# Performance work log

Measured on AMD Instinct MI355X. Metric: run time of the kernel, lower is better.

## Reference

```python
import jax, jax.numpy as jnp
import numpy as np

VOCAB = 32000
DIM = 1024
BATCH = 2
SEQ = 2048
CHUNK = 256
LCTX = 4            # local_context_size, mode='sum'
LOCAL_WIN = 512     # sparse_local_window (>= 2*chunk)
GSTRIDE = 1024      # sparse_global_stride (>= 4*chunk)
LN_EPS = 1e-5


def _cache_positions():
    """Simulate the deterministic sparse KV-cache pruning per chunk (numpy, trace-time).
    Returns list of key-position index arrays (cached positions ++ current chunk)."""
    cache = np.zeros((0,), dtype=np.int64)
    per_chunk = []
    for i in range(SEQ // CHUNK):
        new = np.arange(i * CHUNK, (i + 1) * CHUNK, dtype=np.int64)
        full = np.concatenate([cache, new])
        per_chunk.append(full)
        total_seen = (i + 1) * CHUNK
        local_start = max(0, total_seen - LOCAL_WIN)
        keep = (full >= local_start) | (full % GSTRIDE == 0)
        cache = full[keep]
    return per_chunk


def setup_inputs() -> dict:
    key = jax.random.key(0)
    ks = jax.random.split(key, 8)
    s = 0.02
    return {
        "x": jax.random.randint(ks[0], (BATCH, SEQ), 0, VOCAB, dtype=jnp.int64),
        "emb_table": jax.random.normal(ks[1], (VOCAB, DIM), jnp.float32) * s,
        "q_w": jax.random.normal(ks[2], (DIM, DIM), jnp.float32) * s,
        "q_b": jnp.zeros((DIM,), jnp.float32),
        "k_w": jax.random.normal(ks[3], (DIM, DIM), jnp.float32) * s,
        "k_b": jnp.zeros((DIM,), jnp.float32),
        "v_w": jax.random.normal(ks[4], (DIM, DIM), jnp.float32) * s,
        "v_b": jnp.zeros((DIM,), jnp.float32),
        "o_w": jax.random.normal(ks[5], (DIM, DIM), jnp.float32) * s,
        "o_b": jnp.zeros((DIM,), jnp.float32),
        "ln_w": jnp.ones((DIM,), jnp.float32),
        "ln_b": jnp.zeros((DIM,), jnp.float32),
        "out_w": jax.random.normal(ks[6], (VOCAB, DIM), jnp.float32) * s,
        "out_b": jnp.zeros((VOCAB,), jnp.float32),
    }


def reference(x, emb_table, q_w, q_b, k_w, k_b, v_w, v_b, o_w, o_b, ln_w, ln_b, out_w, out_b):
    # embedding + causal local context (sum of 0..LCTX-1 shifted embeddings)
    emb = emb_table[x]                                  # [B,S,D]
    ctx = emb
    for off in range(1, LCTX):
        ctx = ctx + jnp.pad(emb, ((0, 0), (off, 0), (0, 0)))[:, :SEQ]

    # project full sequence once (same per-chunk projections in the original)
    Q = ctx @ q_w.T + q_b                               # [B,S,D]
    K = ctx @ k_w.T + k_b
    V = ctx @ v_w.T + v_b
    scale = 1.0 / np.sqrt(DIM).astype(np.float32)

    outs = []
    for i, kpos in enumerate(_cache_positions()):
        qpos = np.arange(i * CHUNK, (i + 1) * CHUNK, dtype=np.int64)
        q = Q[:, i * CHUNK:(i + 1) * CHUNK]             # [B,C,D]
        k = K[:, kpos]                                  # [B,Ki,D] gathered sparse cache + chunk
        v = V[:, kpos]
        scores = jnp.einsum('bqd,bkd->bqk', q, k) * scale
        mask = kpos[None, :] > qpos[:, None]            # [C,Ki] static causal mask
        scores = jnp.where(mask[None, :, :], -jnp.inf, scores)
        w = jax.nn.softmax(scores, axis=-1)
        outs.append(jnp.einsum('bqk,bkd->bqd', w, v))

    attended = jnp.concatenate(outs, axis=1)            # [B,S,D]
    h = attended @ o_w.T + o_b
    # LayerNorm
    mu = h.mean(-1, keepdims=True)
    var = ((h - mu) ** 2).mean(-1, keepdims=True)
    h = (h - mu) / jnp.sqrt(var + LN_EPS) * ln_w + ln_b
    return h @ out_w.T + out_b                          # [B,S,VOCAB]
```

## Files before the change

kernel.cpp:

```cpp
#include <hip/hip_runtime.h>
#include <stdint.h>

#define DIMN 1024
#define SEQN 2048
#define BATCHN 2
#define NCHUNK 8
#define CHUNKSZ 256
#define VOCABN 32000
#define ROWS_PB 6016
#define PSTRIDE_B (256*ROWS_PB)
#define LN_EPS 1e-5f

#define MBIG 4096
#define NBIG 32000
#define KBIG 1024
#define NTILES_K (KBIG/64)

typedef unsigned short ushort_t;
typedef __attribute__((ext_vector_type(8))) __bf16 bf16x8;
typedef __attribute__((ext_vector_type(4))) float f32x4;

__device__ const int d_nk[8]   = {256,512,768,769,769,769,769,770};
__device__ const int d_np[8]   = {256,512,768,896,896,896,896,896};
__device__ const int d_koff[8] = {0,256,768,1536,2432,3328,4224,5120};

__device__ __forceinline__ ushort_t f2bu(float f) {
  union { float f; unsigned u; } v; v.f = f;
  unsigned r = v.u + 0x7FFFu + ((v.u >> 16) & 1u);
  return (ushort_t)(r >> 16);
}
__device__ __forceinline__ float b2f(ushort_t u) {
  union { unsigned u; float f; } v; v.u = ((unsigned)u) << 16; return v.f;
}

__device__ __forceinline__ int pos_of(int i, int j) {
  if (i <= 2) return j;
  if (i <= 6) return (j == 0) ? 0 : (i - 3) * 256 + 255 + j;
  return (j == 0) ? 0 : ((j == 1) ? 1024 : 1278 + j);
}

__device__ __forceinline__ void gload16(const void* g, void* l) {
  __builtin_amdgcn_global_load_lds((__attribute__((address_space(1))) void*)g,
                                   (__attribute__((address_space(3))) void*)l,
                                   16, 0, 0);
}

__device__ __forceinline__ void mma_core_s(const ushort_t* __restrict__ A,
                                           const ushort_t* __restrict__ Bt,
                                           int K, ushort_t* lA, ushort_t* lB,
                                           f32x4 acc[4][4], int tid) {
  const int lane = tid & 63;
  const int wr = (tid >> 7) & 1;
  const int wc = (tid >> 6) & 1;
  const int frow = lane & 15;
  const int lhi = lane >> 4;
  const int xk = (frow & 7) << 4;
  const size_t ldb = (size_t)K * 2;
  for (int kt = 0; kt < K; kt += 64) {
#pragma unroll
    for (int t = 0; t < 4; ++t) {
      int cid = t * 256 + tid;
      int row = cid >> 3;
      int srcoff = ((cid & 7) * 16) ^ ((row & 7) << 4);
      gload16((const char*)A  + (size_t)row * ldb + (size_t)kt * 2 + srcoff,
              (char*)lA + cid * 16);
      gload16((const char*)Bt + (size_t)row * ldb + (size_t)kt * 2 + srcoff,
              (char*)lB + cid * 16);
    }
    __syncthreads();
#pragma unroll
    for (int kk = 0; kk < 2; ++kk) {
      bf16x8 af[4], bfr[4];
#pragma unroll
      for (int m = 0; m < 4; ++m) {
        int r = wr * 64 + m * 16 + frow;
        af[m] = *(const bf16x8*)((const char*)lA +
                 ((r * 128 + kk * 64 + lhi * 16) ^ xk));
      }
#pragma unroll
      for (int n = 0; n < 4; ++n) {
        int r = wc * 64 + n * 16 + frow;
        bfr[n] = *(const bf16x8*)((const char*)lB +
                  ((r * 128 + kk * 64 + lhi * 16) ^ xk));
      }
#pragma unroll
      for (int m = 0; m < 4; ++m)
#pragma unroll
        for (int n = 0; n < 4; ++n)
          acc[m][n] = __builtin_amdgcn_mfma_f32_16x16x32_bf16(af[m], bfr[n],
                                                              acc[m][n], 0, 0, 0);
    }
    __syncthreads();
  }
}

__device__ __forceinline__ void stage_tile_big(const char* Abase, const char* Bbase,
                                               ushort_t* ldsbuf, int ktile, int tid) {
  const size_t ldb = (size_t)KBIG * 2;
#pragma unroll
  for (int s = 0; s < 4; ++s) {
    const char* base = (s < 2 ? Abase : Bbase) + (size_t)(s & 1) * 128 * ldb
                       + (size_t)ktile * 128;
    ushort_t* lh = ldsbuf + s * 8192;
#pragma unroll
    for (int r2 = 0; r2 < 2; ++r2) {
      int c = r2 * 512 + tid;
      int row = c >> 3;
      int off_l = (c * 16) ^ ((row & 7) << 4);
      gload16(base + (size_t)row * ldb + (off_l & 127), (char*)lh + c * 16);
    }
  }
}

__global__ __launch_bounds__(512, 2) void k_vocab(
    const ushort_t* __restrict__ A, const ushort_t* __restrict__ Bt,
    const float* __restrict__ bias, float* __restrict__ C) {
  __shared__ ushort_t lds[2][4][8192];
  const int tid = threadIdx.x;
  const int lane = tid & 63, w = tid >> 6, wm = w >> 2, wn = w & 3;
  const int frow = lane & 15, lhi = lane >> 4;
  const int xk = (frow & 7) << 4;

  int l = blockIdx.x;
  int swz = (l & 7) * ((int)gridDim.x >> 3) + (l >> 3);
  const int mt = swz & 15;
  const int nt = swz >> 4;
  const char* Abase = (const char*)(A + (size_t)mt * 256 * KBIG);
  const char* Bbase = (const char*)(Bt + (size_t)nt * 256 * KBIG);

  f32x4 acc[8][4] = {};

  stage_tile_big(Abase, Bbase, &lds[0][0][0], 0, tid);

  for (int kt = 0; kt < NTILES_K; ++kt) {
    const int cur = kt & 1;
    __builtin_amdgcn_sched_barrier(0);
    if (kt + 1 < NTILES_K) {
      stage_tile_big(Abase, Bbase, &lds[cur ^ 1][0][0], kt + 1, tid);
      asm volatile("s_waitcnt vmcnt(8)");
    } else {
      asm volatile("s_waitcnt vmcnt(0)");
    }
    __builtin_amdgcn_s_barrier();
    __builtin_amdgcn_sched_barrier(0);

    const char* lA = (const char*)&lds[cur][wm][0];
    const char* lB = (const char*)&lds[cur][2 + (wn >> 1)][0];

    bf16x8 bF[4][2];
#pragma unroll
    for (int fc = 0; fc < 4; ++fc) {
      int c = (wn & 1) * 64 + fc * 16 + frow;
#pragma unroll
      for (int kk = 0; kk < 2; ++kk)
        bF[fc][kk] = *(const bf16x8*)(lB + ((c * 128 + kk * 64 + lhi * 16) ^ xk));
    }
#pragma unroll
    for (int q = 0; q < 4; ++q) {
      bf16x8 aF[2][2];
#pragma unroll
      for (int i = 0; i < 2; ++i) {
        int r = (2 * q + i) * 16 + frow;
#pragma unroll
        for (int kk = 0; kk < 2; ++kk)
          aF[i][kk] = *(const bf16x8*)(lA + ((r * 128 + kk * 64 + lhi * 16) ^ xk));
      }
      if (q) __builtin_amdgcn_s_barrier();
      __builtin_amdgcn_s_setprio(1);
#pragma unroll
      for (int i = 0; i < 2; ++i)
#pragma unroll
        for (int fc = 0; fc < 4; ++fc)
#pragma unroll
          for (int kk = 0; kk < 2; ++kk)
            acc[2 * q + i][fc] = __builtin_amdgcn_mfma_f32_16x16x32_bf16(
                aF[i][kk], bF[fc][kk], acc[2 * q + i][fc], 0, 0, 0);
      __builtin_amdgcn_s_setprio(0);
    }
    __builtin_amdgcn_s_barrier();
  }

  const int rbase = mt * 256 + wm * 128 + lhi * 4;
  const int cbase = nt * 256 + wn * 64 + frow;
#pragma unroll
  for (int fc = 0; fc < 4; ++fc) {
    float bv = bias[cbase + fc * 16];
#pragma unroll
    for (int fr = 0; fr < 8; ++fr)
#pragma unroll
      for (int j = 0; j < 4; ++j)
        C[(size_t)(rbase + fr * 16 + j) * NBIG + cbase + fc * 16] =
            acc[fr][fc][j] + bv;
  }
}

__global__ __launch_bounds__(256) void k_cvt(const float* __restrict__ src,
                                             ushort_t* __restrict__ dst, int n) {
  int idx = blockIdx.x * 256 + threadIdx.x;
  int stride = gridDim.x * 256;
  int n4 = n >> 2;
  for (int i = idx; i < n4; i += stride) {
    float4 v = ((const float4*)src)[i];
    ((ushort4*)dst)[i] = make_ushort4(f2bu(v.x), f2bu(v.y), f2bu(v.z), f2bu(v.w));
  }
}

__global__ __launch_bounds__(256) void k_embed(const int* __restrict__ x,
                                               const float* __restrict__ emb,
                                               ushort_t* __restrict__ ctxb) {
  const int t = blockIdx.x, b = blockIdx.y, tid = threadIdx.x;
  float4 s = make_float4(0.f, 0.f, 0.f, 0.f);
#pragma unroll
  for (int o = 0; o < 4; ++o) {
    if (t - o < 0) break;
    int tok = x[b * SEQN + t - o];
    float4 v = ((const float4*)(emb + (size_t)tok * DIMN))[tid];
    s.x += v.x; s.y += v.y; s.z += v.z; s.w += v.w;
  }
  ((ushort4*)(ctxb + ((size_t)(b * SEQN + t)) * DIMN))[tid] =
      make_ushort4(f2bu(s.x), f2bu(s.y), f2bu(s.z), f2bu(s.w));
}

__global__ __launch_bounds__(256) void k_qkv(const ushort_t* __restrict__ A,
    const ushort_t* __restrict__ Bt, const float* __restrict__ qb2,
    const float* __restrict__ kb2, const float* __restrict__ vb2,
    ushort_t* __restrict__ Qb, ushort_t* __restrict__ Kb,
    ushort_t* __restrict__ Vb) {
  __shared__ __align__(16) ushort_t lA[128*64];
  __shared__ __align__(16) ushort_t lB[128*64];
  f32x4 acc[4][4] = {};
  const int tid = threadIdx.x;
  mma_core_s(A + (size_t)blockIdx.y * 128 * KBIG,
             Bt + (size_t)blockIdx.x * 128 * KBIG, KBIG, lA, lB, acc, tid);
  const int which = blockIdx.x >> 3;
  const int col0  = (blockIdx.x & 7) * 128;
  ushort_t* Out = (which == 0) ? Qb : (which == 1) ? Kb : Vb;
  const float* Bv = (which == 0) ? qb2 : (which == 1) ? kb2 : vb2;
  const int lane = tid & 63, wr = (tid >> 7) & 1, wc = (tid >> 6) & 1;
  const int rbase = blockIdx.y * 128 + wr * 64 + (lane >> 4) * 4;
  const int cbase = col0 + wc * 64 + (lane & 15);
#pragma unroll
  for (int m = 0; m < 4; ++m)
#pragma unroll
    for (int n = 0; n < 4; ++n) {
      int c = cbase + n * 16;
      float bv = Bv[c];
#pragma unroll
      for (int j = 0; j < 4; ++j)
        Out[(size_t)(rbase + m * 16 + j) * DIMN + c] = f2bu(acc[m][n][j] + bv);
    }
}

__global__ __launch_bounds__(256) void k_gemm_f32(const ushort_t* __restrict__ A,
    const ushort_t* __restrict__ Bt, const float* __restrict__ bias,
    float* __restrict__ C, int N, int K) {
  __shared__ __align__(16) ushort_t lA[128*64];
  __shared__ __align__(16) ushort_t lB[128*64];
  f32x4 acc[4][4] = {};
  const int tid = threadIdx.x;
  mma_core_s(A + (size_t)blockIdx.y * 128 * K, Bt + (size_t)blockIdx.x * 128 * K,
             K, lA, lB, acc, tid);
  const int lane = tid & 63, wr = (tid >> 7) & 1, wc = (tid >> 6) & 1;
  const int rbase = blockIdx.y * 128 + wr * 64 + (lane >> 4) * 4;
  const int cbase = blockIdx.x * 128 + wc * 64 + (lane & 15);
#pragma unroll
  for (int m = 0; m < 4; ++m)
#pragma unroll
    for (int n = 0; n < 4; ++n) {
      int c = cbase + n * 16;
      float bv = bias[c];
#pragma unroll
      for (int j = 0; j < 4; ++j)
        C[(size_t)(rbase + m * 16 + j) * N + c] = acc[m][n][j] + bv;
    }
}

__global__ __launch_bounds__(256) void k_gatherK(const ushort_t* __restrict__ Kb,
                                                 ushort_t* __restrict__ Kg) {
  const int r = blockIdx.x, b = blockIdx.y, tid = threadIdx.x;
  int i = 7;
#pragma unroll
  for (int q = 0; q < 7; ++q) if (r < d_koff[q + 1]) { i = q; break; }
  const int j = r - d_koff[i];
  ushort4* dst = (ushort4*)(Kg + ((size_t)b * ROWS_PB + r) * DIMN);
  if (j < d_nk[i]) {
    int pos = pos_of(i, j);
    dst[tid] = ((const ushort4*)(Kb + ((size_t)b * SEQN + pos) * DIMN))[tid];
  } else {
    dst[tid] = make_ushort4(0, 0, 0, 0);
  }
}

__global__ __launch_bounds__(256) void k_transV(const ushort_t* __restrict__ Vb,
                                                ushort_t* __restrict__ VgT) {
  __shared__ ushort_t tile[64][66];
  const int z = blockIdx.z, b = z >> 3, i = z & 7;
  const int np = d_np[i], nk = d_nk[i], ko = d_koff[i];
  const int jb = blockIdx.x * 64;
  if (jb >= np) return;
  const int db = blockIdx.y * 64;
  const int tid = threadIdx.x, tx = tid & 63, ty = tid >> 6;
#pragma unroll
  for (int rep = 0; rep < 16; ++rep) {
    int jl = rep * 4 + ty;
    int j = jb + jl;
    ushort_t v = 0;
    if (j < nk) v = Vb[((size_t)b * SEQN + pos_of(i, j)) * DIMN + db + tx];
    tile[jl][tx] = v;
  }
  __syncthreads();
  const size_t base = ((size_t)b * ROWS_PB + ko) * DIMN;
#pragma unroll
  for (int rep = 0; rep < 16; ++rep) {
    int dl = rep * 4 + ty;
    VgT[base + (size_t)(db + dl) * np + jb + tx] = tile[tx][dl];
  }
}

__global__ __launch_bounds__(256) void k_scores(const ushort_t* __restrict__ Qb,
    const ushort_t* __restrict__ Kg, ushort_t* __restrict__ P) {
  const int z = blockIdx.z, b = z >> 3, i = z & 7;
  const int np = d_np[i], nk = d_nk[i], ko = d_koff[i];
  if ((int)blockIdx.x * 128 >= np) return;
  __shared__ __align__(16) ushort_t lA[128*64];
  __shared__ __align__(16) ushort_t lB[128*64];
  f32x4 acc[4][4] = {};
  const int tid = threadIdx.x;
  const ushort_t* A  = Qb + ((size_t)(b * SEQN + i * CHUNKSZ) + blockIdx.y * 128) * DIMN;
  const ushort_t* Bt = Kg + ((size_t)b * ROWS_PB + ko + blockIdx.x * 128) * DIMN;
  mma_core_s(A, Bt, DIMN, lA, lB, acc, tid);
  const int lane = tid & 63, wr = (tid >> 7) & 1, wc = (tid >> 6) & 1;
  const int rb = blockIdx.y * 128 + wr * 64 + (lane >> 4) * 4;
  const int cb = blockIdx.x * 128 + wc * 64 + (lane & 15);
  ushort_t* Pc = P + (size_t)b * PSTRIDE_B + (size_t)ko * 256;
  const float scale = 0.03125f;
  const int diag0 = nk - CHUNKSZ;
#pragma unroll
  for (int m = 0; m < 4; ++m)
#pragma unroll
    for (int n = 0; n < 4; ++n) {
      int c = cb + n * 16;
#pragma unroll
      for (int j = 0; j < 4; ++j) {
        int r = rb + m * 16 + j;
        float w = 0.0f;
        if (c < nk && (c - diag0) <= r) w = expf(acc[m][n][j] * scale);
        Pc[(size_t)r * np + c] = f2bu(w);
      }
    }
}

__global__ __launch_bounds__(256) void k_rowsum(const ushort_t* __restrict__ P,
                                                float* __restrict__ rowsum) {
  const int z = blockIdx.y, b = z >> 3, i = z & 7, r = blockIdx.x;
  const int np = d_np[i], ko = d_koff[i];
  const ushort_t* row = P + (size_t)b * PSTRIDE_B + (size_t)ko * 256 + (size_t)r * np;
  const int tid = threadIdx.x;
  float s = 0.f;
  for (int c = tid; c < np; c += 256) s += b2f(row[c]);
#pragma unroll
  for (int o = 1; o < 64; o <<= 1) s += __shfl_xor(s, o);
  __shared__ float ss[4];
  if ((tid & 63) == 0) ss[tid >> 6] = s;
  __syncthreads();
  if (tid == 0) rowsum[z * 256 + r] = ss[0] + ss[1] + ss[2] + ss[3];
}

__global__ __launch_bounds__(256) void k_pv(const ushort_t* __restrict__ P,
    const ushort_t* __restrict__ VgT, const float* __restrict__ rowsum,
    ushort_t* __restrict__ attb) {
  const int z = blockIdx.z, b = z >> 3, i = z & 7;
  const int np = d_np[i], ko = d_koff[i];
  __shared__ __align__(16) ushort_t lA[128*64];
  __shared__ __align__(16) ushort_t lB[128*64];
  f32x4 acc[4][4] = {};
  const int tid = threadIdx.x;
  const ushort_t* A  = P + (size_t)b * PSTRIDE_B + (size_t)ko * 256 +
                       (size_t)blockIdx.y * 128 * np;
  const ushort_t* Bt = VgT + ((size_t)b * ROWS_PB + ko) * DIMN +
                       (size_t)blockIdx.x * 128 * np;
  mma_core_s(A, Bt, np, lA, lB, acc, tid);
  const int lane = tid & 63, wr = (tid >> 7) & 1, wc = (tid >> 6) & 1;
  const int rb = blockIdx.y * 128 + wr * 64 + (lane >> 4) * 4;
  const int cb = blockIdx.x * 128 + wc * 64 + (lane & 15);
  const float* rs = rowsum + z * 256;
  ushort_t* outp = attb + (size_t)(b * SEQN + i * CHUNKSZ) * DIMN;
#pragma unroll
  for (int m = 0; m < 4; ++m)
#pragma unroll
    for (int j = 0; j < 4; ++j) {
      int r = rb + m * 16 + j;
      float inv = 1.0f / rs[r];
#pragma unroll
      for (int n = 0; n < 4; ++n)
        outp[(size_t)r * DIMN + cb + n * 16] = f2bu(acc[m][n][j] * inv);
    }
}

__global__ __launch_bounds__(256) void k_ln(const float* __restrict__ h,
    const float* __restrict__ lnw, const float* __restrict__ lnb,
    ushort_t* __restrict__ hb) {
  const int row = blockIdx.x, tid = threadIdx.x;
  float4 v = ((const float4*)(h + (size_t)row * DIMN))[tid];
  float s  = v.x + v.y + v.z + v.w;
  float sq = v.x * v.x + v.y * v.y + v.z * v.z + v.w * v.w;
#pragma unroll
  for (int o = 1; o < 64; o <<= 1) { s += __shfl_xor(s, o); sq += __shfl_xor(sq, o); }
  __shared__ float ss[4], ssq[4];
  if ((tid & 63) == 0) { ss[tid >> 6] = s; ssq[tid >> 6] = sq; }
  __syncthreads();
  s  = ss[0] + ss[1] + ss[2] + ss[3];
  sq = ssq[0] + ssq[1] + ssq[2] + ssq[3];
  const float mu  = s * (1.0f / DIMN);
  const float var = sq * (1.0f / DIMN) - mu * mu;
  const float inv = rsqrtf(var + LN_EPS);
  float4 w4 = ((const float4*)lnw)[tid];
  float4 b4 = ((const float4*)lnb)[tid];
  ushort4 o4 = make_ushort4(f2bu((v.x - mu) * inv * w4.x + b4.x),
                            f2bu((v.y - mu) * inv * w4.y + b4.y),
                            f2bu((v.z - mu) * inv * w4.z + b4.z),
                            f2bu((v.w - mu) * inv * w4.w + b4.w));
  ((ushort4*)(hb + (size_t)row * DIMN))[tid] = o4;
}

extern "C" void kernel_launch(void* const* d_in, const int* in_sizes, int n_in,
                              void* d_out, int out_size, void* d_ws, size_t ws_size,
                              hipStream_t stream) {
  const int*   x    = (const int*)  d_in[0];
  const float* emb  = (const float*)d_in[1];
  const float* qw   = (const float*)d_in[2];
  const float* qb   = (const float*)d_in[3];
  const float* kw   = (const float*)d_in[4];
  const float* kb   = (const float*)d_in[5];
  const float* vw   = (const float*)d_in[6];
  const float* vb   = (const float*)d_in[7];
  const float* ow   = (const float*)d_in[8];
  const float* ob   = (const float*)d_in[9];
  const float* lnw  = (const float*)d_in[10];
  const float* lnb  = (const float*)d_in[11];
  const float* outw = (const float*)d_in[12];
  const float* outb = (const float*)d_in[13];
  float* out = (float*)d_out;
  (void)in_sizes; (void)n_in; (void)out_size; (void)ws_size;

  char* ws = (char*)d_ws;
  size_t off = 0;
  auto alloc = [&](size_t bytes) {
    size_t r = off; off += (bytes + 255) & ~(size_t)255; return r;
  };
  ushort_t* wqkvb = (ushort_t*)(ws + alloc((size_t)3 * DIMN * DIMN * 2));
  ushort_t* wob   = (ushort_t*)(ws + alloc((size_t)DIMN * DIMN * 2));
  ushort_t* woutb = (ushort_t*)(ws + alloc((size_t)VOCABN * DIMN * 2));
  ushort_t* ctxb  = (ushort_t*)(ws + alloc((size_t)BATCHN * SEQN * DIMN * 2));
  ushort_t* Qb    = (ushort_t*)(ws + alloc((size_t)BATCHN * SEQN * DIMN * 2));
  ushort_t* Kb    = (ushort_t*)(ws + alloc((size_t)BATCHN * SEQN * DIMN * 2));
  ushort_t* Vb    = (ushort_t*)(ws + alloc((size_t)BATCHN * SEQN * DIMN * 2));
  ushort_t* Kg    = (ushort_t*)(ws + alloc((size_t)BATCHN * ROWS_PB * DIMN * 2));
  ushort_t* VgT   = (ushort_t*)(ws + alloc((size_t)BATCHN * ROWS_PB * DIMN * 2));
  ushort_t* Pm    = (ushort_t*)(ws + alloc((size_t)BATCHN * PSTRIDE_B * 2));
  float*    rsum  = (float*)   (ws + alloc((size_t)BATCHN * NCHUNK * 256 * 4));
  ushort_t* attb  = (ushort_t*)(ws + alloc((size_t)BATCHN * SEQN * DIMN * 2));
  float*    hbuf  = (float*)   (ws + alloc((size_t)BATCHN * SEQN * DIMN * 4));
  ushort_t* hb    = (ushort_t*)(ws + alloc((size_t)BATCHN * SEQN * DIMN * 2));

  k_cvt<<<dim3(1024), dim3(256), 0, stream>>>(qw, wqkvb,                 DIMN * DIMN);
  k_cvt<<<dim3(1024), dim3(256), 0, stream>>>(kw, wqkvb + DIMN * DIMN,   DIMN * DIMN);
  k_cvt<<<dim3(1024), dim3(256), 0, stream>>>(vw, wqkvb + 2 * DIMN * DIMN, DIMN * DIMN);
  k_cvt<<<dim3(1024), dim3(256), 0, stream>>>(ow,   wob,   DIMN * DIMN);
  k_cvt<<<dim3(2048), dim3(256), 0, stream>>>(outw, woutb, VOCABN * DIMN);

  k_embed<<<dim3(SEQN, BATCHN), dim3(256), 0, stream>>>(x, emb, ctxb);

  k_qkv<<<dim3(24, 32), dim3(256), 0, stream>>>(ctxb, wqkvb, qb, kb, vb,
                                                Qb, Kb, Vb);

  k_gatherK<<<dim3(ROWS_PB, BATCHN), dim3(256), 0, stream>>>(Kb, Kg);
  k_transV<<<dim3(14, 16, BATCHN * NCHUNK), dim3(256), 0, stream>>>(Vb, VgT);

  k_scores<<<dim3(7, 2, BATCHN * NCHUNK), dim3(256), 0, stream>>>(Qb, Kg, Pm);
  k_rowsum<<<dim3(256, BATCHN * NCHUNK), dim3(256), 0, stream>>>(Pm, rsum);
  k_pv<<<dim3(8, 2, BATCHN * NCHUNK), dim3(256), 0, stream>>>(Pm, VgT, rsum, attb);

  k_gemm_f32<<<dim3(8, 32), dim3(256), 0, stream>>>(attb, wob, ob, hbuf, DIMN, DIMN);
  k_ln<<<dim3(BATCHN * SEQN), dim3(256), 0, stream>>>(hbuf, lnw, lnb, hb);

  k_vocab<<<dim3(2000), dim3(512), 0, stream>>>(hb, woutb, outb, out);
}
```

Measured before the change: 604.4 us.

## Split vocab GEMM into 256-tile and 128-tile kernels; store o-proj output in bf16

The vocab projection now runs as two launches. A 256x256-tile kernel covers the first 16128 vocab columns, and a 128x128-tile kernel covers the remaining columns. The aim is to rebalance the tile count against the CU count and reduce wave-quantization tail effects. Separately, the output projection now writes bf16 instead of fp32 and LayerNorm reads bf16, which halves that intermediate's memory traffic at the cost of rounding h before normalization. The smaller tiles in the second vocab kernel get less data reuse per tile and add a kernel boundary.

```diff
diff --git a/kernel.cpp b/kernel.cpp
--- a/kernel.cpp
+++ b/kernel.cpp
@@ -15,6 +15,7 @@
 #define NBIG 32000
 #define KBIG 1024
 #define NTILES_K (KBIG/64)
+#define NSPLIT 16128
 
 typedef unsigned short ushort_t;
 typedef __attribute__((ext_vector_type(8))) __bf16 bf16x8;
@@ -112,7 +113,7 @@
   }
 }
 
-__global__ __launch_bounds__(512, 2) void k_vocab(
+__global__ __launch_bounds__(512, 2) void k_vocab256(
     const ushort_t* __restrict__ A, const ushort_t* __restrict__ Bt,
     const float* __restrict__ bias, float* __restrict__ C) {
   __shared__ ushort_t lds[2][4][8192];
@@ -192,6 +193,35 @@
         C[(size_t)(rbase + fr * 16 + j) * NBIG + cbase + fc * 16] =
             acc[fr][fc][j] + bv;
   }
+}
+
+__global__ __launch_bounds__(256) void k_vocab128s(
+    const ushort_t* __restrict__ A, const ushort_t* __restrict__ Bt,
+    const float* __restrict__ bias, float* __restrict__ C) {
+  int l = blockIdx.x;
+  int swz = (l & 7) * ((int)gridDim.x >> 3) + (l >> 3);
+  const int mt = swz & 31;
+  const int nt = swz >> 5;
+  const int col0 = NSPLIT + nt * 128;
+  __shared__ __align__(16) ushort_t lA[128*64];
+  __shared__ __align__(16) ushort_t lB[128*64];
+  f32x4 acc[4][4] = {};
+  const int tid = threadIdx.x;
+  mma_core_s(A + (size_t)mt * 128 * KBIG, Bt + (size_t)col0 * KBIG,
+             KBIG, lA, lB, acc, tid);
+  const int lane = tid & 63, wr = (tid >> 7) & 1, wc = (tid >> 6) & 1;
+  const int rbase = mt * 128 + wr * 64 + (lane >> 4) * 4;
+  const int cbase = col0 + wc * 64 + (lane & 15);
+#pragma unroll
+  for (int m = 0; m < 4; ++m)
+#pragma unroll
+    for (int n = 0; n < 4; ++n) {
+      int c = cbase + n * 16;
+      float bv = bias[c];
+#pragma unroll
+      for (int j = 0; j < 4; ++j)
+        C[(size_t)(rbase + m * 16 + j) * NBIG + c] = acc[m][n][j] + bv;
+    }
 }
 
 __global__ __launch_bounds__(256) void k_cvt(const float* __restrict__ src,
@@ -251,15 +281,15 @@
     }
 }
 
-__global__ __launch_bounds__(256) void k_gemm_f32(const ushort_t* __restrict__ A,
+__global__ __launch_bounds__(256) void k_oproj(const ushort_t* __restrict__ A,
     const ushort_t* __restrict__ Bt, const float* __restrict__ bias,
-    float* __restrict__ C, int N, int K) {
+    ushort_t* __restrict__ C) {
   __shared__ __align__(16) ushort_t lA[128*64];
   __shared__ __align__(16) ushort_t lB[128*64];
   f32x4 acc[4][4] = {};
   const int tid = threadIdx.x;
-  mma_core_s(A + (size_t)blockIdx.y * 128 * K, Bt + (size_t)blockIdx.x * 128 * K,
-             K, lA, lB, acc, tid);
+  mma_core_s(A + (size_t)blockIdx.y * 128 * KBIG,
+             Bt + (size_t)blockIdx.x * 128 * KBIG, KBIG, lA, lB, acc, tid);
   const int lane = tid & 63, wr = (tid >> 7) & 1, wc = (tid >> 6) & 1;
   const int rbase = blockIdx.y * 128 + wr * 64 + (lane >> 4) * 4;
   const int cbase = blockIdx.x * 128 + wc * 64 + (lane & 15);
@@ -271,7 +301,7 @@
       float bv = bias[c];
 #pragma unroll
       for (int j = 0; j < 4; ++j)
-        C[(size_t)(rbase + m * 16 + j) * N + c] = acc[m][n][j] + bv;
+        C[(size_t)(rbase + m * 16 + j) * DIMN + c] = f2bu(acc[m][n][j] + bv);
     }
 }
 
@@ -397,11 +427,12 @@
     }
 }
 
-__global__ __launch_bounds__(256) void k_ln(const float* __restrict__ h,
+__global__ __launch_bounds__(256) void k_ln(const ushort_t* __restrict__ h,
     const float* __restrict__ lnw, const float* __restrict__ lnb,
     ushort_t* __restrict__ hb) {
   const int row = blockIdx.x, tid = threadIdx.x;
-  float4 v = ((const float4*)(h + (size_t)row * DIMN))[tid];
+  ushort4 u4 = ((const ushort4*)(h + (size_t)row * DIMN))[tid];
+  float4 v = make_float4(b2f(u4.x), b2f(u4.y), b2f(u4.z), b2f(u4.w));
   float s  = v.x + v.y + v.z + v.w;
   float sq = v.x * v.x + v.y * v.y + v.z * v.z + v.w * v.w;
 #pragma unroll
@@ -460,7 +491,7 @@
   ushort_t* Pm    = (ushort_t*)(ws + alloc((size_t)BATCHN * PSTRIDE_B * 2));
   float*    rsum  = (float*)   (ws + alloc((size_t)BATCHN * NCHUNK * 256 * 4));
   ushort_t* attb  = (ushort_t*)(ws + alloc((size_t)BATCHN * SEQN * DIMN * 2));
-  float*    hbuf  = (float*)   (ws + alloc((size_t)BATCHN * SEQN * DIMN * 4));
+  ushort_t* hbuf  = (ushort_t*)(ws + alloc((size_t)BATCHN * SEQN * DIMN * 2));
   ushort_t* hb    = (ushort_t*)(ws + alloc((size_t)BATCHN * SEQN * DIMN * 2));
 
   k_cvt<<<dim3(1024), dim3(256), 0, stream>>>(qw, wqkvb,                 DIMN * DIMN);
@@ -481,8 +512,9 @@
   k_rowsum<<<dim3(256, BATCHN * NCHUNK), dim3(256), 0, stream>>>(Pm, rsum);
   k_pv<<<dim3(8, 2, BATCHN * NCHUNK), dim3(256), 0, stream>>>(Pm, VgT, rsum, attb);
 
-  k_gemm_f32<<<dim3(8, 32), dim3(256), 0, stream>>>(attb, wob, ob, hbuf, DIMN, DIMN);
+  k_oproj<<<dim3(8, 32), dim3(256), 0, stream>>>(attb, wob, ob, hbuf);
   k_ln<<<dim3(BATCHN * SEQN), dim3(256), 0, stream>>>(hbuf, lnw, lnb, hb);
 
-  k_vocab<<<dim3(2000), dim3(512), 0, stream>>>(hb, woutb, outb, out);
-}
+  k_vocab256<<<dim3(1008), dim3(512), 0, stream>>>(hb, woutb, outb, out);
+  k_vocab128s<<<dim3(3968), dim3(256), 0, stream>>>(hb, woutb, outb, out);
+}
```

Result: slower. 690.4 us (+14.2%).
